# Optimization experiments

Hardware: AMD Instinct MI355X
Metric: run time of the kernel (lower is better)

## Reference

```python
import jax, jax.numpy as jnp
import numpy as np
from jax import lax

C = 128
B, H, W = 8, 128, 128
HW = H * W


def _layernorm(x, w, b):
    # x: [b,c,h,w]; WithBias LN over channel dim c (matches to_3d -> LN(last dim=c) -> to_4d)
    mu = jnp.mean(x, axis=1, keepdims=True)
    var = jnp.mean((x - mu) ** 2, axis=1, keepdims=True)
    xn = (x - mu) / jnp.sqrt(var + 1e-5)
    return xn * w[None, :, None, None] + b[None, :, None, None]


def _conv1x1(x, w, b):
    # x: [b,c,h,w], w: [out,in]
    return jnp.einsum('bchw,oc->bohw', x, w) + b[None, :, None, None]


def _dwconv3(x, w, b):
    # depthwise 3x3, w: [c,1,3,3]
    c = x.shape[1]
    y = lax.conv_general_dilated(x, w, window_strides=(1, 1),
                                 padding=((1, 1), (1, 1)),
                                 feature_group_count=c,
                                 dimension_numbers=('NCHW', 'OIHW', 'NCHW'))
    return y + b[None, :, None, None]


def _l2norm(x):
    # torch F.normalize(dim=-1): x / max(||x||, 1e-12)
    n = jnp.sqrt(jnp.sum(x * x, axis=-1, keepdims=True))
    return x / jnp.maximum(n, 1e-12)


def setup_inputs() -> dict:
    key = jax.random.key(0)
    ks = jax.random.split(key, 12)
    s = 0.02
    return {
        'pre': jax.random.normal(ks[0], (B, HW, C), jnp.float32),
        'cur': jax.random.normal(ks[1], (B, HW, C), jnp.float32),
        'ln1_w': jnp.ones((C,), jnp.float32),
        'ln1_b': jnp.zeros((C,), jnp.float32),
        'ln2_w': jnp.ones((C,), jnp.float32),
        'ln2_b': jnp.zeros((C,), jnp.float32),
        'q_w1': jax.random.normal(ks[2], (C, C), jnp.float32) * s,
        'q_b1': jnp.zeros((C,), jnp.float32),
        'q_w2': jax.random.normal(ks[3], (C, 1, 3, 3), jnp.float32) * s,
        'q_b2': jnp.zeros((C,), jnp.float32),
        'kv_w1': jax.random.normal(ks[4], (2 * C, C), jnp.float32) * s,
        'kv_b1': jnp.zeros((2 * C,), jnp.float32),
        'kv_w2': jax.random.normal(ks[5], (2 * C, 1, 3, 3), jnp.float32) * s,
        'kv_b2': jnp.zeros((2 * C,), jnp.float32),
        'out_w': jax.random.normal(ks[6], (C, C), jnp.float32) * s,
        'out_b': jnp.zeros((C,), jnp.float32),
    }


def reference(pre, cur, ln1_w, ln1_b, ln2_w, ln2_b,
              q_w1, q_b1, q_w2, q_b2,
              kv_w1, kv_b1, kv_w2, kv_b2,
              out_w, out_b):
    b, hw, c = cur.shape
    h = w = int(np.sqrt(hw))
    # [b,hw,c] -> [b,c,h,w]
    cur4 = jnp.transpose(cur.reshape(b, h, w, c), (0, 3, 1, 2))
    pre4 = jnp.transpose(pre.reshape(b, h, w, c), (0, 3, 1, 2))

    pre_ln = _layernorm(pre4, ln1_w, ln1_b)
    cur_ln = _layernorm(cur4, ln2_w, ln2_b)

    q = _dwconv3(_conv1x1(cur_ln, q_w1, q_b1), q_w2, q_b2)        # [b,c,h,w]
    kv = _dwconv3(_conv1x1(pre_ln, kv_w1, kv_b1), kv_w2, kv_b2)   # [b,2c,h,w]
    k, v = jnp.split(kv, 2, axis=1)

    q = _l2norm(q.reshape(b, c, hw))
    k = _l2norm(k.reshape(b, c, hw))
    v = v.reshape(b, c, hw)

    att = jax.nn.softmax(jnp.einsum('bcn,bdn->bcd', q, k), axis=-1)  # [b,c,c]
    out = jnp.einsum('bcd,bdn->bcn', att, v).reshape(b, c, h, w)

    out = _conv1x1(out, out_w, out_b) + cur4                         # residual
    # [b,c,h,w] -> [b,hw,c]
    return jnp.transpose(out.reshape(b, c, hw), (0, 2, 1))
```

## Files before the change

### kernel.cpp

```cpp
#include <hip/hip_runtime.h>

typedef __attribute__((ext_vector_type(4))) float f32x4;
typedef __attribute__((ext_vector_type(2))) float f32x2;
typedef __attribute__((ext_vector_type(8))) short s16x8;
typedef __attribute__((ext_vector_type(4))) short s16x4;
typedef __bf16 bf16x8 __attribute__((ext_vector_type(8)));

__device__ __forceinline__ short f2bf(float f) {
  union { float f; unsigned u; } c; c.f = f;
  unsigned r = c.u + 0x7fffu + ((c.u >> 16) & 1u);
  return (short)(r >> 16);
}
__device__ __forceinline__ float bf2f(short s) {
  union { unsigned u; float f; } c; c.u = ((unsigned)(unsigned short)s) << 16;
  return c.f;
}

__global__ void k0_prep(const float* __restrict__ qw1, const float* __restrict__ qb1,
                        const float* __restrict__ kvw1, const float* __restrict__ kvb1,
                        const float* __restrict__ ln1w, const float* __restrict__ ln1b,
                        const float* __restrict__ ln2w, const float* __restrict__ ln2b,
                        short* __restrict__ Wq, short* __restrict__ Wk, short* __restrict__ Wv,
                        float* __restrict__ T)
{
  const int path = blockIdx.x;
  const int o = threadIdx.x >> 1, hf = threadIdx.x & 1;
  const float *W, *bias, *lw, *lb; short* Wo; float *t1, *t2;
  if (path == 0)      { W = qw1;            bias = qb1;       lw = ln2w; lb = ln2b; Wo = Wq; t1 = T;       t2 = T + 128; }
  else if (path == 1) { W = kvw1;           bias = kvb1;      lw = ln1w; lb = ln1b; Wo = Wk; t1 = T + 256; t2 = T + 384; }
  else                { W = kvw1 + 16384;   bias = kvb1+128;  lw = ln1w; lb = ln1b; Wo = Wv; t1 = T + 512; t2 = T + 640; }
  float s1 = 0.f, s2 = 0.f;
  for (int g = 0; g < 64; g++) {
    const int c = hf * 64 + g;
    const float w = W[o * 128 + c];
    const float wp = w * lw[c];
    s1 += wp; s2 += w * lb[c];
    Wo[o * 128 + c] = f2bf(wp);
  }
  s1 += __shfl_xor(s1, 1);
  s2 += __shfl_xor(s2, 1);
  if (hf == 0) { t1[o] = s1; t2[o] = s2 + bias[o]; }
}

__device__ __forceinline__ void k1_loadR(const float* __restrict__ src, f32x4 (&PR)[16])
{
#pragma unroll
  for (int g = 0; g < 8; g++) {
    PR[2 * g]     = *(const f32x4*)(src + g * 8);
    PR[2 * g + 1] = *(const f32x4*)(src + g * 8 + 4);
  }
}

__device__ __forceinline__ void k1_stageW(const f32x4 (&PR)[16], int tid,
                                          short (&At)[128][136], f32x2 (&rowstat)[128])
{
  const int r = tid >> 1, hf = tid & 1;
  float s1 = 0.f, s2 = 0.f;
#pragma unroll
  for (int g = 0; g < 8; g++) {
    const f32x4 v0 = PR[2 * g];
    const f32x4 v1 = PR[2 * g + 1];
    s16x8 o;
#pragma unroll
    for (int j = 0; j < 4; j++) {
      s1 += v0[j] + v1[j]; s2 += v0[j] * v0[j] + v1[j] * v1[j];
      o[j] = f2bf(v0[j]); o[4 + j] = f2bf(v1[j]);
    }
    *(s16x8*)&At[r][hf * 64 + g * 8] = o;
  }
  s1 += __shfl_xor(s1, 1);
  s2 += __shfl_xor(s2, 1);
  if (hf == 0) {
    const float mu = s1 * (1.f / 128.f);
    const float var = s2 * (1.f / 128.f) - mu * mu;
    rowstat[r] = (f32x2){mu, rsqrtf(var + 1e-5f)};
  }
}

__device__ __forceinline__ void k1_gemm_epi(const short (&At)[128][136],
                                            const f32x2 (&rowstat)[128],
                                            const short* __restrict__ Wp,
                                            const float* __restrict__ t1,
                                            const float* __restrict__ t2,
                                            short* __restrict__ Yout,
                                            int b, int pl0,
                                            int wv, int l16, int quad, int kof)
{
  f32x4 acc[2][8];
#pragma unroll
  for (int i = 0; i < 2; i++)
#pragma unroll
    for (int j = 0; j < 8; j++) acc[i][j] = (f32x4){0.f, 0.f, 0.f, 0.f};

#pragma unroll
  for (int ks = 0; ks < 4; ks++) {
    const int kb = ks * 32 + kof;
    const bf16x8 a0 = *(const bf16x8*)&At[wv * 32 + l16][kb];
    const bf16x8 a1 = *(const bf16x8*)&At[wv * 32 + 16 + l16][kb];
#pragma unroll
    for (int j = 0; j < 8; j++) {
      const bf16x8 bv = *(const bf16x8*)(Wp + (j * 16 + l16) * 128 + kb);
      acc[0][j] = __builtin_amdgcn_mfma_f32_16x16x32_bf16(a0, bv, acc[0][j], 0, 0, 0);
      acc[1][j] = __builtin_amdgcn_mfma_f32_16x16x32_bf16(a1, bv, acc[1][j], 0, 0, 0);
    }
  }
  float t1v[8], t2v[8];
#pragma unroll
  for (int j = 0; j < 8; j++) { const int o = j * 16 + l16; t1v[j] = t1[o]; t2v[j] = t2[o]; }
#pragma unroll
  for (int i = 0; i < 2; i++) {
    const int pr = wv * 32 + i * 16 + quad * 4;
    f32x2 st[4];
#pragma unroll
    for (int rg = 0; rg < 4; rg++) st[rg] = rowstat[pr + rg];
#pragma unroll
    for (int j = 0; j < 8; j++) {
      const int o = j * 16 + l16;
      s16x4 pk;
#pragma unroll
      for (int rg = 0; rg < 4; rg++) {
        const float y = st[rg].y * acc[i][j][rg] - st[rg].x * st[rg].y * t1v[j] + t2v[j];
        pk[rg] = f2bf(y);
      }
      *(s16x4*)(Yout + ((size_t)(b * 128 + o)) * 16384 + pl0 + pr) = pk;
    }
  }
}

__global__ __launch_bounds__(256, 3)
void k1_ln_gemm(const float* __restrict__ cur, const float* __restrict__ pre,
                const short* __restrict__ Wq, const short* __restrict__ Wk,
                const short* __restrict__ Wv, const float* __restrict__ T,
                short* __restrict__ Yq, short* __restrict__ Yk, short* __restrict__ Yv)
{
  __shared__ __attribute__((aligned(16))) short At[128][136];
  __shared__ f32x2 rowstat[128];
  const int tid = threadIdx.x, bx = blockIdx.x;
  const int path = bx >> 9;
  const int m0 = (bx & 511) * 2;
  const float* X = (path == 0) ? cur : pre;
  const short* Wp = (path == 0) ? Wq : (path == 1) ? Wk : Wv;
  short* Yout = (path == 0) ? Yq : (path == 1) ? Yk : Yv;
  const float* t1 = T + path * 256;
  const float* t2 = t1 + 128;
  const int wv = tid >> 6, lane = tid & 63, l16 = lane & 15, quad = lane >> 4, kof = quad * 8;
  const int r = tid >> 1, hf = tid & 1;
  const float* src0 = X + ((size_t)(m0 * 128 + r)) * 128 + hf * 64;

  f32x4 PR[16];
  k1_loadR(src0, PR);
  k1_stageW(PR, tid, At, rowstat);
  __syncthreads();
  k1_loadR(src0 + 16384, PR);
  k1_gemm_epi(At, rowstat, Wp, t1, t2, Yout, m0 >> 7, (m0 & 127) * 128,
              wv, l16, quad, kof);
  __syncthreads();
  k1_stageW(PR, tid, At, rowstat);
  __syncthreads();
  k1_gemm_epi(At, rowstat, Wp, t1, t2, Yout, (m0 + 1) >> 7, ((m0 + 1) & 127) * 128,
              wv, l16, quad, kof);
}

__global__ __launch_bounds__(256, 4)
void k2_plane(const short* __restrict__ Yq, const short* __restrict__ Yk,
              const short* __restrict__ Yv,
              const float* __restrict__ qw2, const float* __restrict__ qb2,
              const float* __restrict__ kvw2, const float* __restrict__ kvb2,
              short* __restrict__ qo, short* __restrict__ ko, short* __restrict__ vo,
              float* __restrict__ nq, float* __restrict__ nk)
{
  __shared__ __attribute__((aligned(16))) short tile[130][144];
  __shared__ float red[256];
  const int tid = threadIdx.x, bx = blockIdx.x;
  const int path = bx >> 10, rem = bx & 1023;
  const int b = rem >> 7, c = rem & 127;
  const short* in; const float* w2p; float bsv; short* outp; float* np;
  if (path == 0)      { in = Yq; w2p = qw2 + c * 9;          bsv = qb2[c];        outp = qo; np = nq; }
  else if (path == 1) { in = Yk; w2p = kvw2 + c * 9;         bsv = kvb2[c];       outp = ko; np = nk; }
  else                { in = Yv; w2p = kvw2 + (128 + c) * 9; bsv = kvb2[128 + c]; outp = vo; np = nullptr; }

  const short* plane = in + ((size_t)(b * 128 + c)) * 16384;
#pragma unroll
  for (int g = 0; g < 8; g++) {
    const int e = (g * 256 + tid) * 8;
    *(s16x8*)&tile[(e >> 7) + 1][(e & 127) + 8] = *(const s16x8*)(plane + e);
  }
  const s16x8 z8 = (s16x8){0, 0, 0, 0, 0, 0, 0, 0};
  if (tid < 128) *(s16x8*)&tile[tid + 1][136] = z8;
  if (tid < 36) { const int rr = (tid / 18) * 129, cc = (tid % 18) * 8; *(s16x8*)&tile[rr][cc] = z8; }
  __syncthreads();

  float wt[9];
#pragma unroll
  for (int j = 0; j < 9; j++) wt[j] = w2p[j];
  const int rr = tid >> 1, hfc = tid & 1;

  float A0[8], A1[8], A2[8];
  {
    const int ca = 8 + hfc * 64;
    const s16x8 a0 = *(const s16x8*)&tile[rr][ca];
    const s16x8 a1 = *(const s16x8*)&tile[rr + 1][ca];
    const s16x8 a2 = *(const s16x8*)&tile[rr + 2][ca];
#pragma unroll
    for (int x = 0; x < 8; x++) { A0[x] = bf2f(a0[x]); A1[x] = bf2f(a1[x]); A2[x] = bf2f(a2[x]); }
  }
  float p0, p1, p2;
  if (hfc) { p0 = bf2f(tile[rr][71]); p1 = bf2f(tile[rr + 1][71]); p2 = bf2f(tile[rr + 2][71]); }
  else { p0 = p1 = p2 = 0.f; }

  float ss = 0.f;
  short* oplane = outp + ((size_t)(b * 128 + c)) * 16384 + rr * 128 + hfc * 64;
#pragma unroll
  for (int g = 0; g < 8; g++) {
    const int cb = 16 + hfc * 64 + g * 8;
    const s16x8 b0 = *(const s16x8*)&tile[rr][cb];
    const s16x8 b1 = *(const s16x8*)&tile[rr + 1][cb];
    const s16x8 b2 = *(const s16x8*)&tile[rr + 2][cb];
    float B0[8], B1[8], B2[8];
#pragma unroll
    for (int x = 0; x < 8; x++) { B0[x] = bf2f(b0[x]); B1[x] = bf2f(b1[x]); B2[x] = bf2f(b2[x]); }
    s16x8 ov;
#pragma unroll
    for (int x = 0; x < 8; x++) {
      const float l0 = x ? A0[x - 1] : p0, l1 = x ? A1[x - 1] : p1, l2 = x ? A2[x - 1] : p2;
      const float r0 = (x < 7) ? A0[x + 1] : B0[0];
      const float r1 = (x < 7) ? A1[x + 1] : B1[0];
      const float r2 = (x < 7) ? A2[x + 1] : B2[0];
      float s = bsv;
      s += wt[0] * l0 + wt[1] * A0[x] + wt[2] * r0;
      s += wt[3] * l1 + wt[4] * A1[x] + wt[5] * r1;
      s += wt[6] * l2 + wt[7] * A2[x] + wt[8] * r2;
      ov[x] = f2bf(s); ss += s * s;
    }
    *(s16x8*)(oplane + g * 8) = ov;
    p0 = A0[7]; p1 = A1[7]; p2 = A2[7];
#pragma unroll
    for (int x = 0; x < 8; x++) { A0[x] = B0[x]; A1[x] = B1[x]; A2[x] = B2[x]; }
  }
  red[tid] = ss;
  __syncthreads();
  if (tid < 64) {
    float t = red[tid] + red[tid + 64] + red[tid + 128] + red[tid + 192];
#pragma unroll
    for (int m = 32; m >= 1; m >>= 1) t += __shfl_xor(t, m);
    if (tid == 0 && np) np[b * 128 + c] = t;
  }
}

__global__ __launch_bounds__(256, 2)
void k3_gram(const short* __restrict__ qo, const short* __restrict__ ko,
             float* __restrict__ Gp)
{
  const int tid = threadIdx.x, bx = blockIdx.x;
  const int b = bx >> 6, sp = bx & 63;
  const int wv = tid >> 6, lane = tid & 63, l16 = lane & 15, quad = lane >> 4, kof = quad * 8;
  f32x4 acc[2][8];
#pragma unroll
  for (int i = 0; i < 2; i++)
#pragma unroll
    for (int j = 0; j < 8; j++) acc[i][j] = (f32x4){0.f, 0.f, 0.f, 0.f};

  const short* qb = qo + (size_t)b * 128 * 16384 + sp * 256 + kof;
  const short* kb = ko + (size_t)b * 128 * 16384 + sp * 256 + kof;
#pragma unroll
  for (int ks = 0; ks < 8; ks++) {
    const int n0 = ks * 32;
    const bf16x8 a0 = *(const bf16x8*)(qb + (size_t)(wv * 32 + l16) * 16384 + n0);
    const bf16x8 a1 = *(const bf16x8*)(qb + (size_t)(wv * 32 + 16 + l16) * 16384 + n0);
#pragma unroll
    for (int j = 0; j < 8; j++) {
      const bf16x8 bv = *(const bf16x8*)(kb + (size_t)(j * 16 + l16) * 16384 + n0);
      acc[0][j] = __builtin_amdgcn_mfma_f32_16x16x32_bf16(a0, bv, acc[0][j], 0, 0, 0);
      acc[1][j] = __builtin_amdgcn_mfma_f32_16x16x32_bf16(a1, bv, acc[1][j], 0, 0, 0);
    }
  }
  float* gp = Gp + ((size_t)(sp * 8 + b)) * 16384;
#pragma unroll
  for (int i = 0; i < 2; i++)
#pragma unroll
    for (int j = 0; j < 8; j++)
#pragma unroll
      for (int rg = 0; rg < 4; rg++)
        gp[(wv * 32 + i * 16 + quad * 4 + rg) * 128 + j * 16 + l16] = acc[i][j][rg];
}

__global__ void k4a_softmax(const float* __restrict__ Gp,
                            const float* __restrict__ nq, const float* __restrict__ nk,
                            float* __restrict__ att)
{
  const int tid = threadIdx.x;
  const int b = blockIdx.x >> 5;
  const int c = (blockIdx.x & 31) * 4 + (tid >> 6);
  const int lane = tid & 63;
  const int d0 = lane * 2;
  f32x2 a = (f32x2){0.f, 0.f};
  for (int ks = 0; ks < 64; ks++)
    a += *(const f32x2*)(Gp + ((size_t)(ks * 8 + b)) * 16384 + c * 128 + d0);
  const float qn = fmaxf(sqrtf(nq[b * 128 + c]), 1e-12f);
  const f32x2 nk2 = *(const f32x2*)(nk + b * 128 + d0);
  f32x2 sc;
  sc[0] = a[0] / (qn * fmaxf(sqrtf(nk2[0]), 1e-12f));
  sc[1] = a[1] / (qn * fmaxf(sqrtf(nk2[1]), 1e-12f));
  float mx = fmaxf(sc[0], sc[1]);
#pragma unroll
  for (int m = 32; m >= 1; m >>= 1) mx = fmaxf(mx, __shfl_xor(mx, m));
  f32x2 e; float sum;
  e[0] = __expf(sc[0] - mx); e[1] = __expf(sc[1] - mx);
  sum = e[0] + e[1];
#pragma unroll
  for (int m = 32; m >= 1; m >>= 1) sum += __shfl_xor(sum, m);
  const float inv = 1.f / sum;
  f32x2 o; o[0] = e[0] * inv; o[1] = e[1] * inv;
  *(f32x2*)(att + (size_t)b * 16384 + c * 128 + d0) = o;
}

__global__ void k4b_mw(const float* __restrict__ att, const float* __restrict__ outw,
                       short* __restrict__ Mb)
{
  __shared__ float at[128][8];
  const int tid = threadIdx.x, bx = blockIdx.x;
  const int b = bx >> 4, d0 = (bx & 15) * 8;
  {
    const int cc = tid >> 1, q = tid & 1;
    *(f32x4*)&at[cc][q * 4] = *(const f32x4*)(att + (size_t)b * 16384 + cc * 128 + d0 + q * 4);
  }
  __syncthreads();
  const int o = tid & 127, dq = (tid >> 7) * 4;
  f32x4 acc = (f32x4){0.f, 0.f, 0.f, 0.f};
  const float* wr = outw + o * 128;
  for (int cc = 0; cc < 128; cc++) {
    const float w = wr[cc];
    const f32x4 a = *(const f32x4*)&at[cc][dq];
    acc += w * a;
  }
  s16x4 pk;
#pragma unroll
  for (int rg = 0; rg < 4; rg++) pk[rg] = f2bf(acc[rg]);
  *(s16x4*)(Mb + ((size_t)(b * 128 + o)) * 128 + d0 + dq) = pk;
}

__global__ __launch_bounds__(256, 3)
void k5_out(const short* __restrict__ Mb, const short* __restrict__ vp,
            const float* __restrict__ outb, const float* __restrict__ cur,
            float* __restrict__ out)
{
  __shared__ __attribute__((aligned(16))) short Vt[128][136];
  const int tid = threadIdx.x;
  const int b = blockIdx.x >> 7, nb = (blockIdx.x & 127) * 128;
  {
    const int d = tid >> 1, hf = tid & 1;
    const short* src = vp + ((size_t)(b * 128 + d)) * 16384 + nb + hf * 64;
#pragma unroll
    for (int g = 0; g < 8; g++) {
      const s16x8 v = *(const s16x8*)(src + g * 8);
#pragma unroll
      for (int x = 0; x < 8; x++) Vt[hf * 64 + g * 8 + x][d] = v[x];
    }
  }
  __syncthreads();
  const int wv = tid >> 6, lane = tid & 63, l16 = lane & 15, quad = lane >> 4, kof = quad * 8;
  f32x4 acc[2][8];
#pragma unroll
  for (int i = 0; i < 2; i++)
#pragma unroll
    for (int j = 0; j < 8; j++) acc[i][j] = (f32x4){0.f, 0.f, 0.f, 0.f};

  const short* m0 = Mb + ((size_t)(b * 128 + wv * 32 + l16)) * 128;
  const short* m1 = m0 + 16 * 128;
#pragma unroll
  for (int ks = 0; ks < 4; ks++) {
    const int kb = ks * 32 + kof;
    const bf16x8 a0 = *(const bf16x8*)(m0 + kb);
    const bf16x8 a1 = *(const bf16x8*)(m1 + kb);
#pragma unroll
    for (int j = 0; j < 8; j++) {
      const bf16x8 bv = *(const bf16x8*)&Vt[j * 16 + l16][kb];
      acc[0][j] = __builtin_amdgcn_mfma_f32_16x16x32_bf16(a0, bv, acc[0][j], 0, 0, 0);
      acc[1][j] = __builtin_amdgcn_mfma_f32_16x16x32_bf16(a1, bv, acc[1][j], 0, 0, 0);
    }
  }
#pragma unroll
  for (int i = 0; i < 2; i++) {
    const int o0 = wv * 32 + i * 16 + quad * 4;
    const f32x4 bias = *(const f32x4*)(outb + o0);
#pragma unroll
    for (int j = 0; j < 8; j++) {
      const int pos = nb + j * 16 + l16;
      const size_t idx = ((size_t)(b * 16384 + pos)) * 128 + o0;
      const f32x4 cv = *(const f32x4*)(cur + idx);
      f32x4 rr;
#pragma unroll
      for (int rg = 0; rg < 4; rg++) rr[rg] = acc[i][j][rg] + bias[rg] + cv[rg];
      *(f32x4*)(out + idx) = rr;
    }
  }
}

extern "C" void kernel_launch(void* const* d_in, const int* in_sizes, int n_in,
                              void* d_out, int out_size, void* d_ws, size_t ws_size,
                              hipStream_t stream) {
  const float* pre  = (const float*)d_in[0];
  const float* cur  = (const float*)d_in[1];
  const float* ln1w = (const float*)d_in[2];
  const float* ln1b = (const float*)d_in[3];
  const float* ln2w = (const float*)d_in[4];
  const float* ln2b = (const float*)d_in[5];
  const float* qw1  = (const float*)d_in[6];
  const float* qb1  = (const float*)d_in[7];
  const float* qw2  = (const float*)d_in[8];
  const float* qb2  = (const float*)d_in[9];
  const float* kvw1 = (const float*)d_in[10];
  const float* kvb1 = (const float*)d_in[11];
  const float* kvw2 = (const float*)d_in[12];
  const float* kvb2 = (const float*)d_in[13];
  const float* outw = (const float*)d_in[14];
  const float* outb = (const float*)d_in[15];

  char* ws = (char*)d_ws;
  short* Yq  = (short*)(ws);
  short* Yk  = (short*)(ws + 33554432);
  short* Yv  = (short*)(ws + 67108864);
  short* qo  = (short*)(ws + 100663296);
  short* ko  = (short*)(ws + 134217728);
  short* vo  = (short*)(ws + 167772160);
  float* Gp  = (float*)(ws);
  float* att = (float*)(ws + 33554432);
  short* Mb  = (short*)(ws + 34078720);
  char*  sm  = ws + 201326592;
  short* Wq  = (short*)(sm);
  short* Wk  = (short*)(sm + 32768);
  short* Wv  = (short*)(sm + 65536);
  float* T   = (float*)(sm + 98304);
  float* nq  = (float*)(sm + 102400);
  float* nk  = (float*)(sm + 106496);

  hipLaunchKernelGGL(k0_prep, dim3(3), dim3(256), 0, stream,
                     qw1, qb1, kvw1, kvb1, ln1w, ln1b, ln2w, ln2b, Wq, Wk, Wv, T);
  hipLaunchKernelGGL(k1_ln_gemm, dim3(1536), dim3(256), 0, stream,
                     cur, pre, Wq, Wk, Wv, T, Yq, Yk, Yv);
  hipLaunchKernelGGL(k2_plane, dim3(3072), dim3(256), 0, stream,
                     Yq, Yk, Yv, qw2, qb2, kvw2, kvb2, qo, ko, vo, nq, nk);
  hipLaunchKernelGGL(k3_gram, dim3(512), dim3(256), 0, stream, qo, ko, Gp);
  hipLaunchKernelGGL(k4a_softmax, dim3(256), dim3(256), 0, stream, Gp, nq, nk, att);
  hipLaunchKernelGGL(k4b_mw, dim3(128), dim3(256), 0, stream, att, outw, Mb);
  hipLaunchKernelGGL(k5_out, dim3(1024), dim3(256), 0, stream, Mb, vo, outb, cur, (float*)d_out);
}
```

Before: 426.3 us.

## Stage bf16 weights in LDS for LN+GEMM kernel, one tile per block

The LN+1x1-conv GEMM kernel now copies the 128x128 bf16 weight matrix into shared memory once per block and reads B fragments from LDS instead of global memory. The two-tile software pipeline (prefetching the next tile into registers while computing the current one) is removed, so each block handles one 128-row tile and the grid doubles to 3072 blocks. The aim is to cut repeated global/L2 weight fetches inside the MFMA loop. In exchange it adds LDS footprint (lower occupancy bound of 2), a weight-load prologue per tile, and loses the load/compute overlap.

```diff
diff --git a/kernel.cpp b/kernel.cpp
--- a/kernel.cpp
+++ b/kernel.cpp
@@ -42,50 +42,60 @@
   if (hf == 0) { t1[o] = s1; t2[o] = s2 + bias[o]; }
 }
 
-__device__ __forceinline__ void k1_loadR(const float* __restrict__ src, f32x4 (&PR)[16])
-{
-#pragma unroll
-  for (int g = 0; g < 8; g++) {
-    PR[2 * g]     = *(const f32x4*)(src + g * 8);
-    PR[2 * g + 1] = *(const f32x4*)(src + g * 8 + 4);
-  }
-}
-
-__device__ __forceinline__ void k1_stageW(const f32x4 (&PR)[16], int tid,
-                                          short (&At)[128][136], f32x2 (&rowstat)[128])
-{
-  const int r = tid >> 1, hf = tid & 1;
-  float s1 = 0.f, s2 = 0.f;
-#pragma unroll
-  for (int g = 0; g < 8; g++) {
-    const f32x4 v0 = PR[2 * g];
-    const f32x4 v1 = PR[2 * g + 1];
-    s16x8 o;
-#pragma unroll
-    for (int j = 0; j < 4; j++) {
-      s1 += v0[j] + v1[j]; s2 += v0[j] * v0[j] + v1[j] * v1[j];
-      o[j] = f2bf(v0[j]); o[4 + j] = f2bf(v1[j]);
-    }
-    *(s16x8*)&At[r][hf * 64 + g * 8] = o;
-  }
-  s1 += __shfl_xor(s1, 1);
-  s2 += __shfl_xor(s2, 1);
-  if (hf == 0) {
-    const float mu = s1 * (1.f / 128.f);
-    const float var = s2 * (1.f / 128.f) - mu * mu;
-    rowstat[r] = (f32x2){mu, rsqrtf(var + 1e-5f)};
-  }
-}
-
-__device__ __forceinline__ void k1_gemm_epi(const short (&At)[128][136],
-                                            const f32x2 (&rowstat)[128],
-                                            const short* __restrict__ Wp,
-                                            const float* __restrict__ t1,
-                                            const float* __restrict__ t2,
-                                            short* __restrict__ Yout,
-                                            int b, int pl0,
-                                            int wv, int l16, int quad, int kof)
-{
+__global__ __launch_bounds__(256, 2)
+void k1_ln_gemm(const float* __restrict__ cur, const float* __restrict__ pre,
+                const short* __restrict__ Wq, const short* __restrict__ Wk,
+                const short* __restrict__ Wv, const float* __restrict__ T,
+                short* __restrict__ Yq, short* __restrict__ Yk, short* __restrict__ Yv)
+{
+  __shared__ __attribute__((aligned(16))) short At[128][144];
+  __shared__ __attribute__((aligned(16))) short Wl[128][144];
+  __shared__ f32x2 rowstat[128];
+  const int tid = threadIdx.x, bx = blockIdx.x;
+  const int path = bx >> 10;
+  const int mblk = bx & 1023;
+  const float* X = (path == 0) ? cur : pre;
+  const short* Wp = (path == 0) ? Wq : (path == 1) ? Wk : Wv;
+  short* Yout = (path == 0) ? Yq : (path == 1) ? Yk : Yv;
+  const float* t1 = T + path * 256;
+  const float* t2 = t1 + 128;
+  const int b = mblk >> 7;
+  const int pl0 = (mblk & 127) * 128;
+
+  {
+    const int o = tid >> 1, hf = tid & 1;
+    const short* src = Wp + o * 128 + hf * 64;
+#pragma unroll
+    for (int g = 0; g < 8; g++)
+      *(s16x8*)&Wl[o][hf * 64 + g * 8] = *(const s16x8*)(src + g * 8);
+  }
+  {
+    const int r = tid >> 1, hf = tid & 1;
+    const float* src = X + ((size_t)(mblk * 128 + r)) * 128 + hf * 64;
+    float s1 = 0.f, s2 = 0.f;
+#pragma unroll
+    for (int g = 0; g < 8; g++) {
+      const f32x4 v0 = *(const f32x4*)(src + g * 8);
+      const f32x4 v1 = *(const f32x4*)(src + g * 8 + 4);
+      s16x8 o;
+#pragma unroll
+      for (int j = 0; j < 4; j++) {
+        s1 += v0[j] + v1[j]; s2 += v0[j] * v0[j] + v1[j] * v1[j];
+        o[j] = f2bf(v0[j]); o[4 + j] = f2bf(v1[j]);
+      }
+      *(s16x8*)&At[r][hf * 64 + g * 8] = o;
+    }
+    s1 += __shfl_xor(s1, 1);
+    s2 += __shfl_xor(s2, 1);
+    if (hf == 0) {
+      const float mu = s1 * (1.f / 128.f);
+      const float var = s2 * (1.f / 128.f) - mu * mu;
+      rowstat[r] = (f32x2){mu, rsqrtf(var + 1e-5f)};
+    }
+  }
+  __syncthreads();
+
+  const int wv = tid >> 6, lane = tid & 63, l16 = lane & 15, quad = lane >> 4, kof = quad * 8;
   f32x4 acc[2][8];
 #pragma unroll
   for (int i = 0; i < 2; i++)
@@ -99,11 +109,12 @@
     const bf16x8 a1 = *(const bf16x8*)&At[wv * 32 + 16 + l16][kb];
 #pragma unroll
     for (int j = 0; j < 8; j++) {
-      const bf16x8 bv = *(const bf16x8*)(Wp + (j * 16 + l16) * 128 + kb);
+      const bf16x8 bv = *(const bf16x8*)&Wl[j * 16 + l16][kb];
       acc[0][j] = __builtin_amdgcn_mfma_f32_16x16x32_bf16(a0, bv, acc[0][j], 0, 0, 0);
       acc[1][j] = __builtin_amdgcn_mfma_f32_16x16x32_bf16(a1, bv, acc[1][j], 0, 0, 0);
     }
   }
+
   float t1v[8], t2v[8];
 #pragma unroll
   for (int j = 0; j < 8; j++) { const int o = j * 16 + l16; t1v[j] = t1[o]; t2v[j] = t2[o]; }
@@ -125,40 +136,6 @@
       *(s16x4*)(Yout + ((size_t)(b * 128 + o)) * 16384 + pl0 + pr) = pk;
     }
   }
-}
-
-__global__ __launch_bounds__(256, 3)
-void k1_ln_gemm(const float* __restrict__ cur, const float* __restrict__ pre,
-                const short* __restrict__ Wq, const short* __restrict__ Wk,
-                const short* __restrict__ Wv, const float* __restrict__ T,
-                short* __restrict__ Yq, short* __restrict__ Yk, short* __restrict__ Yv)
-{
-  __shared__ __attribute__((aligned(16))) short At[128][136];
-  __shared__ f32x2 rowstat[128];
-  const int tid = threadIdx.x, bx = blockIdx.x;
-  const int path = bx >> 9;
-  const int m0 = (bx & 511) * 2;
-  const float* X = (path == 0) ? cur : pre;
-  const short* Wp = (path == 0) ? Wq : (path == 1) ? Wk : Wv;
-  short* Yout = (path == 0) ? Yq : (path == 1) ? Yk : Yv;
-  const float* t1 = T + path * 256;
-  const float* t2 = t1 + 128;
-  const int wv = tid >> 6, lane = tid & 63, l16 = lane & 15, quad = lane >> 4, kof = quad * 8;
-  const int r = tid >> 1, hf = tid & 1;
-  const float* src0 = X + ((size_t)(m0 * 128 + r)) * 128 + hf * 64;
-
-  f32x4 PR[16];
-  k1_loadR(src0, PR);
-  k1_stageW(PR, tid, At, rowstat);
-  __syncthreads();
-  k1_loadR(src0 + 16384, PR);
-  k1_gemm_epi(At, rowstat, Wp, t1, t2, Yout, m0 >> 7, (m0 & 127) * 128,
-              wv, l16, quad, kof);
-  __syncthreads();
-  k1_stageW(PR, tid, At, rowstat);
-  __syncthreads();
-  k1_gemm_epi(At, rowstat, Wp, t1, t2, Yout, (m0 + 1) >> 7, ((m0 + 1) & 127) * 128,
-              wv, l16, quad, kof);
 }
 
 __global__ __launch_bounds__(256, 4)
@@ -436,7 +413,7 @@
 
   hipLaunchKernelGGL(k0_prep, dim3(3), dim3(256), 0, stream,
                      qw1, qb1, kvw1, kvb1, ln1w, ln1b, ln2w, ln2b, Wq, Wk, Wv, T);
-  hipLaunchKernelGGL(k1_ln_gemm, dim3(1536), dim3(256), 0, stream,
+  hipLaunchKernelGGL(k1_ln_gemm, dim3(3072), dim3(256), 0, stream,
                      cur, pre, Wq, Wk, Wv, T, Yq, Yk, Yv);
   hipLaunchKernelGGL(k2_plane, dim3(3072), dim3(256), 0, stream,
                      Yq, Yk, Yv, qw2, qb2, kvw2, kvb2, qo, ko, vo, nq, nk);
```

Result: faster. 386.5 us (-9.3%).
